# Kernel optimization log

Measured on AMD Instinct MI355X. Metric: run time of the kernel, lower is better.

## Reference

```python
import jax, jax.numpy as jnp
import numpy as np

B, C, H, W = 16, 512, 32, 32
G = min(C // 4, 32)  # group-norm groups = 32
EPS = 1e-6


def setup_inputs() -> dict:
    key = jax.random.key(0)
    ks = jax.random.split(key, 9)
    s = 1.0 / np.sqrt(C)
    return {
        "x": jax.random.normal(ks[0], (B, C, H, W), dtype=jnp.float32),
        "gn_gamma": jnp.ones((C,), jnp.float32),
        "gn_beta": jnp.zeros((C,), jnp.float32),
        "W0": jax.random.normal(ks[1], (C, C), jnp.float32) * s,
        "b0": jnp.zeros((C,), jnp.float32),
        "W1": jax.random.normal(ks[2], (C, C), jnp.float32) * s,
        "b1": jnp.zeros((C,), jnp.float32),
        "W2": jax.random.normal(ks[3], (C, C), jnp.float32) * s,
        "b2": jnp.zeros((C,), jnp.float32),
        "W3": jax.random.normal(ks[4], (C, C), jnp.float32) * s,
        "b3": jnp.zeros((C,), jnp.float32),
    }


def _group_norm(x, gamma, beta):
    b, c, h, w = x.shape
    xg = x.reshape(b, G, c // G, h, w)
    mu = jnp.mean(xg, axis=(2, 3, 4), keepdims=True)
    var = jnp.var(xg, axis=(2, 3, 4), keepdims=True)
    xn = ((xg - mu) * jax.lax.rsqrt(var + EPS)).reshape(b, c, h, w)
    return xn * gamma[None, :, None, None] + beta[None, :, None, None]


def _nin(x, Wm, bv):
    # 1x1 conv via channel contraction: bchw,cd->bdhw
    return jnp.einsum('bchw,cd->bdhw', x, Wm) + bv[None, :, None, None]


def reference(x, gn_gamma, gn_beta, W0, b0, W1, b1, W2, b2, W3, b3):
    b, c, h, w = x.shape
    hn = _group_norm(x, gn_gamma, gn_beta)
    q = _nin(hn, W0, b0)
    k = _nin(hn, W1, b1)
    v = _nin(hn, W2, b2)
    # attention scores over all spatial positions: [b, h, w, i, j]
    scores = jnp.einsum('bchw,bcij->bhwij', q, k) * (c ** -0.5)
    attn = jax.nn.softmax(scores.reshape(b, h, w, h * w), axis=-1).reshape(b, h, w, h, w)
    o = jnp.einsum('bhwij,bcij->bchw', attn, v)
    o = _nin(o, W3, b3)
    return x + o  # skip_rescale=False
```

## Files before the change

kernel.cpp:

```cpp
#include <hip/hip_runtime.h>
#include <stdint.h>

typedef __bf16 bf16_t;
typedef _Float16 f16_t;
typedef bf16_t bf16x8 __attribute__((ext_vector_type(8)));
typedef bf16_t bf16x4 __attribute__((ext_vector_type(4)));
typedef f16_t  f16x8  __attribute__((ext_vector_type(8)));
typedef f16_t  f16x4  __attribute__((ext_vector_type(4)));
typedef float floatx4 __attribute__((ext_vector_type(4)));

static constexpr int NB  = 16;
static constexpr int NC  = 512;
static constexpr int NHW = 1024;
static constexpr int NG  = 32;
static constexpr int CPG = 16;

#define SCALE 0.044194173824159216f
#define LOG2E 1.4426950408889634f

__global__ __launch_bounds__(256) void gn_stats_k(const float* __restrict__ x,
                                                  float* __restrict__ stats) {
  int bg = blockIdx.x;
  const float* xp = x + (size_t)bg * CPG * NHW;
  float s = 0.f, ss = 0.f;
  for (int i = threadIdx.x * 4; i < CPG * NHW; i += 256 * 4) {
    float4 v = *(const float4*)&xp[i];
    s += v.x + v.y + v.z + v.w;
    ss += v.x * v.x + v.y * v.y + v.z * v.z + v.w * v.w;
  }
#pragma unroll
  for (int off = 1; off < 64; off <<= 1) {
    s  += __shfl_xor(s,  off, 64);
    ss += __shfl_xor(ss, off, 64);
  }
  __shared__ float red[2][4];
  int wv = threadIdx.x >> 6;
  if ((threadIdx.x & 63) == 0) { red[0][wv] = s; red[1][wv] = ss; }
  __syncthreads();
  if (threadIdx.x == 0) {
    float st  = red[0][0] + red[0][1] + red[0][2] + red[0][3];
    float sst = red[1][0] + red[1][1] + red[1][2] + red[1][3];
    float mean = st * (1.f / 16384.f);
    float var  = sst * (1.f / 16384.f) - mean * mean;
    stats[bg * 2]     = mean;
    stats[bg * 2 + 1] = rsqrtf(var + 1e-6f);
  }
}

__global__ __launch_bounds__(256) void gn_apply_k(const float* __restrict__ x,
                                                  const float* __restrict__ gamma,
                                                  const float* __restrict__ beta,
                                                  const float* __restrict__ stats,
                                                  bf16_t* __restrict__ hnT,
                                                  bf16_t* __restrict__ hnN) {
  int bi = blockIdx.z;
  int c0 = blockIdx.y * 32;
  int n0 = blockIdx.x * 32;
  __shared__ float tile[32][33];
  int tn = threadIdx.x & 31;
  int tr = threadIdx.x >> 5;
  const float* xb = x + (size_t)bi * NC * NHW;
#pragma unroll
  for (int r = 0; r < 4; r++) {
    int c = c0 + tr + r * 8;
    int g = c >> 4;
    float mean = stats[(bi * NG + g) * 2];
    float rstd = stats[(bi * NG + g) * 2 + 1];
    float ga = gamma[c], be = beta[c];
    float v = xb[(size_t)c * NHW + n0 + tn];
    tile[tr + r * 8][tn] = (v - mean) * rstd * ga + be;
  }
  __syncthreads();
  int rl = threadIdx.x >> 3, ch = (threadIdx.x & 7) * 4;
  bf16_t* hb = hnT + (size_t)bi * NHW * NC;
  bf16x4 pk;
#pragma unroll
  for (int i = 0; i < 4; i++) pk[i] = (bf16_t)tile[ch + i][rl];
  *(bf16x4*)&hb[(size_t)(n0 + rl) * NC + c0 + ch] = pk;
  bf16_t* hc = hnN + (size_t)bi * NC * NHW;
  bf16x4 pk2;
#pragma unroll
  for (int i = 0; i < 4; i++) pk2[i] = (bf16_t)tile[rl][ch + i];
  *(bf16x4*)&hc[(size_t)(c0 + rl) * NHW + n0 + ch] = pk2;
}

__global__ __launch_bounds__(256) void wprep1_k(const float* __restrict__ W0,
                                                const float* __restrict__ W1,
                                                const float* __restrict__ W2,
                                                const float* __restrict__ W3,
                                                const float* __restrict__ b0,
                                                const float* __restrict__ b2,
                                                const float* __restrict__ b3,
                                                bf16_t* __restrict__ Wt,
                                                float* __restrict__ u,
                                                float* __restrict__ bb) {
  int z = blockIdx.z;
  if (z < 3) {
    const float* W = (z == 0) ? W0 : (z == 1) ? W1 : W2;
    bf16_t* o = Wt + (size_t)z * NC * NC;
    int d0 = blockIdx.x * 32, c0 = blockIdx.y * 32;
    int cl = threadIdx.x >> 3, dc = (threadIdx.x & 7) * 4;
    float4 v = *(const float4*)&W[(size_t)(c0 + cl) * NC + d0 + dc];
    bf16x4 pk;
    pk[0] = (bf16_t)v.x; pk[1] = (bf16_t)v.y; pk[2] = (bf16_t)v.z; pk[3] = (bf16_t)v.w;
    *(bf16x4*)&o[(size_t)(c0 + cl) * NC + d0 + dc] = pk;
    return;
  }
  if (z == 3) {
    bf16_t* o = Wt + (size_t)3 * NC * NC;
    int d0 = blockIdx.x * 32, c0 = blockIdx.y * 32;
    __shared__ float tile[32][33];
    int tdx = threadIdx.x & 31, tr = threadIdx.x >> 5;
#pragma unroll
    for (int r = 0; r < 4; r++)
      tile[tr + r * 8][tdx] = W3[(size_t)(c0 + tr + r * 8) * NC + d0 + tdx];
    __syncthreads();
    int dl = threadIdx.x >> 3, cc = (threadIdx.x & 7) * 4;
    bf16x4 pk;
#pragma unroll
    for (int i = 0; i < 4; i++) pk[i] = (bf16_t)tile[cc + i][dl];
    *(bf16x4*)&o[(size_t)(d0 + dl) * NC + c0 + cc] = pk;
    return;
  }
  int bx = blockIdx.x, by = blockIdx.y;
  if (by < 8) {
    int cblock = by * 16 + bx;
    int wv = threadIdx.x >> 6, lane = threadIdx.x & 63;
    int c = cblock * 4 + wv;
    const float* wr = W1 + (size_t)c * NC + lane * 8;
    float s = 0.f;
#pragma unroll
    for (int k = 0; k < 8; k++) s += wr[k] * b0[lane * 8 + k];
#pragma unroll
    for (int off = 1; off < 64; off <<= 1) s += __shfl_xor(s, off, 64);
    if (lane == 0) u[c] = SCALE * s;
    return;
  }
  if (by == 8 && bx < 8) {
    int e0 = bx * 64;
    int el = threadIdx.x & 63, sl = threadIdx.x >> 6;
    float s = 0.f;
    for (int d = sl * 128; d < sl * 128 + 128; d++)
      s += b2[d] * W3[(size_t)d * NC + e0 + el];
    __shared__ float red[4][64];
    red[sl][el] = s;
    __syncthreads();
    if (threadIdx.x < 64)
      bb[e0 + threadIdx.x] = red[0][threadIdx.x] + red[1][threadIdx.x] +
                             red[2][threadIdx.x] + red[3][threadIdx.x] + b3[e0 + threadIdx.x];
  }
}

__global__ __launch_bounds__(256) void w_k(const bf16_t* __restrict__ hnT,
                                           const float* __restrict__ u,
                                           float* __restrict__ w) {
  int row = blockIdx.x * 4 + (threadIdx.x >> 6);
  int lane = threadIdx.x & 63;
  bf16x8 h = *(const bf16x8*)&hnT[(size_t)row * NC + lane * 8];
  const float* up = u + lane * 8;
  float s = 0.f;
#pragma unroll
  for (int k = 0; k < 8; k++) s += (float)h[k] * up[k];
#pragma unroll
  for (int off = 1; off < 64; off <<= 1) s += __shfl_xor(s, off, 64);
  if (lane == 0) w[row] = s;
}

__device__ __forceinline__ void glds16(const bf16_t* g, bf16_t* lds) {
  __builtin_amdgcn_global_load_lds(
      (const __attribute__((address_space(1))) unsigned int*)g,
      (__attribute__((address_space(3))) unsigned int*)lds, 16, 0, 0);
}

__device__ __forceinline__ floatx4 mfma_bf16(bf16x8 a, bf16x8 b, floatx4 c) {
  return __builtin_amdgcn_mfma_f32_16x16x32_bf16(a, b, c, 0, 0, 0);
}

template<int KDIM, bool SWAP>
__device__ __forceinline__ void gemm_core(const bf16_t* __restrict__ A,
                                          const bf16_t* __restrict__ B,
                                          int m0, int n0,
                                          floatx4 (&acc)[4][4]) {
  __shared__ bf16_t As[128 * 64];
  __shared__ bf16_t Bs[128 * 64];
  const int tid = threadIdx.x, lane = tid & 63, wv = tid >> 6;
  const int l16 = lane & 15, quad = lane >> 4;
  const int wm = wv & 1, wn = wv >> 1;
  const int x7 = l16 & 7;

  const int srow = lane >> 3;
  const int schunk = (lane & 7) ^ srow;
  const bf16_t* aptr = A + (size_t)(m0 + wv * 32 + srow) * KDIM + schunk * 8;
  const bf16_t* bptr = B + (size_t)(n0 + wv * 32 + srow) * KDIM + schunk * 8;
  bf16_t* as_ = &As[(wv * 32) * 64];
  bf16_t* bs_ = &Bs[(wv * 32) * 64];

  for (int k0 = 0; k0 < KDIM; k0 += 64) {
    __syncthreads();
#pragma unroll
    for (int i = 0; i < 4; i++) {
      glds16(aptr + (size_t)(8 * i) * KDIM, as_ + (8 * i) * 64);
      glds16(bptr + (size_t)(8 * i) * KDIM, bs_ + (8 * i) * 64);
    }
    aptr += 64; bptr += 64;
    __syncthreads();
    bf16x8 af[2][4], bfv[2][4];
#pragma unroll
    for (int h = 0; h < 2; h++)
#pragma unroll
      for (int i = 0; i < 4; i++) {
        int q = h * 4 + quad;
        af[h][i]  = *(const bf16x8*)&As[(wm * 64 + i * 16 + l16) * 64 + ((q ^ x7) * 8)];
        bfv[h][i] = *(const bf16x8*)&Bs[(wn * 64 + i * 16 + l16) * 64 + ((q ^ x7) * 8)];
      }
#pragma unroll
    for (int h = 0; h < 2; h++)
#pragma unroll
      for (int i = 0; i < 4; i++)
#pragma unroll
        for (int j = 0; j < 4; j++)
          acc[i][j] = SWAP ? mfma_bf16(bfv[h][j], af[h][i], acc[i][j])
                           : mfma_bf16(af[h][i], bfv[h][j], acc[i][j]);
  }
}

#define ACC_INIT(acc)                                   \
  floatx4 acc[4][4];                                    \
  _Pragma("unroll") for (int i = 0; i < 4; i++)         \
  _Pragma("unroll") for (int j = 0; j < 4; j++)         \
    acc[i][j] = (floatx4){0.f, 0.f, 0.f, 0.f};

__global__ __launch_bounds__(256) void wprep2_k(const bf16_t* __restrict__ Wt,
                                                bf16_t* __restrict__ Mt,
                                                bf16_t* __restrict__ W23t) {
  int z = blockIdx.z;
  const bf16_t* A = (z == 0) ? (Wt + (size_t)1 * NC * NC) : (Wt + (size_t)3 * NC * NC);
  const bf16_t* B = (z == 0) ? (Wt + (size_t)0 * NC * NC) : (Wt + (size_t)2 * NC * NC);
  bf16_t* out = (z == 0) ? Mt : W23t;
  const float sc = (z == 0) ? SCALE : 1.f;
  int n0 = blockIdx.x * 128, m0 = blockIdx.y * 128;
  ACC_INIT(acc);
  gemm_core<NC, false>(A, B, m0, n0, acc);
  const int lane = threadIdx.x & 63, wv = threadIdx.x >> 6;
  const int l16 = lane & 15, quad = lane >> 4, wm = wv & 1, wn = wv >> 1;
#pragma unroll
  for (int i = 0; i < 4; i++)
#pragma unroll
    for (int j = 0; j < 4; j++) {
      int row = m0 + wm * 64 + i * 16 + quad * 4;
      int col = n0 + wn * 64 + j * 16 + l16;
#pragma unroll
      for (int r = 0; r < 4; r++)
        out[(size_t)(row + r) * NC + col] = (bf16_t)(acc[i][j][r] * sc);
    }
}

__global__ __launch_bounds__(256) void gemm_g_k(const bf16_t* __restrict__ hnT,
                                                const bf16_t* __restrict__ Mt,
                                                bf16_t* __restrict__ G) {
  int n0 = blockIdx.x * 128, m0 = blockIdx.y * 128;
  ACC_INIT(acc);
  gemm_core<NC, true>(hnT, Mt, m0, n0, acc);
  const int lane = threadIdx.x & 63, wv = threadIdx.x >> 6;
  const int l16 = lane & 15, quad = lane >> 4, wm = wv & 1, wn = wv >> 1;
#pragma unroll
  for (int i = 0; i < 4; i++) {
    int m = m0 + wm * 64 + i * 16 + l16;
#pragma unroll
    for (int j = 0; j < 4; j++) {
      int eb = n0 + wn * 64 + j * 16 + quad * 4;
      bf16x4 pk;
#pragma unroll
      for (int r = 0; r < 4; r++) pk[r] = (bf16_t)(acc[i][j][r]);
      *(bf16x4*)&G[(size_t)m * NC + eb] = pk;
    }
  }
}

__global__ __launch_bounds__(256) void gemm_s_k(const bf16_t* __restrict__ G,
                                                const bf16_t* __restrict__ hnT,
                                                f16_t* __restrict__ S) {
  int bi = blockIdx.z;
  int n0 = blockIdx.x * 128, m0 = blockIdx.y * 128;
  const bf16_t* A = G + (size_t)bi * NHW * NC;
  const bf16_t* B = hnT + (size_t)bi * NHW * NC;
  ACC_INIT(acc);
  gemm_core<NC, true>(A, B, m0, n0, acc);

  const int lane = threadIdx.x & 63, wv = threadIdx.x >> 6;
  const int l16 = lane & 15, quad = lane >> 4, wm = wv & 1, wn = wv >> 1;
  f16_t* out = S + (size_t)bi * NHW * NHW;
#pragma unroll
  for (int i = 0; i < 4; i++) {
    int m = m0 + wm * 64 + i * 16 + l16;
#pragma unroll
    for (int j = 0; j < 4; j++) {
      int nb = n0 + wn * 64 + j * 16 + quad * 4;
      f16x4 pk;
#pragma unroll
      for (int r = 0; r < 4; r++) pk[r] = (f16_t)(acc[i][j][r]);
      *(f16x4*)&out[(size_t)m * NHW + nb] = pk;
    }
  }
}

__global__ __launch_bounds__(256) void softmax_k(const f16_t* __restrict__ S,
                                                 const float* __restrict__ w,
                                                 bf16_t* __restrict__ P) {
  int row = blockIdx.x * 4 + (threadIdx.x >> 6);
  int lane = threadIdx.x & 63;
  int b = row >> 10;
  const f16_t* sp = S + (size_t)row * NHW + lane * 16;
  const float* wp = w + b * NHW + lane * 16;
  f16x8 a = *(const f16x8*)sp;
  f16x8 bq = *(const f16x8*)(sp + 8);
  float v[16];
#pragma unroll
  for (int k = 0; k < 8; k++) { v[k] = (float)a[k] + wp[k]; v[8 + k] = (float)bq[k] + wp[8 + k]; }
  float mx = v[0];
#pragma unroll
  for (int k = 1; k < 16; k++) mx = fmaxf(mx, v[k]);
#pragma unroll
  for (int off = 1; off < 64; off <<= 1) mx = fmaxf(mx, __shfl_xor(mx, off, 64));
  float e[16], s = 0.f;
#pragma unroll
  for (int k = 0; k < 16; k++) { e[k] = exp2f((v[k] - mx) * LOG2E); s += e[k]; }
#pragma unroll
  for (int off = 1; off < 64; off <<= 1) s += __shfl_xor(s, off, 64);
  float inv = 1.f / s;
  bf16x8 o0, o1;
#pragma unroll
  for (int k = 0; k < 8; k++) { o0[k] = (bf16_t)(e[k] * inv); o1[k] = (bf16_t)(e[8 + k] * inv); }
  bf16_t* pp = P + (size_t)row * NHW + lane * 16;
  *(bf16x8*)pp = o0;
  *(bf16x8*)(pp + 8) = o1;
}

__global__ __launch_bounds__(256) void gemm_t_k(const bf16_t* __restrict__ P,
                                                const bf16_t* __restrict__ hnN,
                                                bf16_t* __restrict__ T) {
  int bi = blockIdx.z;
  int n0 = blockIdx.x * 128, m0 = blockIdx.y * 128;
  const bf16_t* A = P + (size_t)bi * NHW * NHW;
  const bf16_t* B = hnN + (size_t)bi * NC * NHW;
  ACC_INIT(acc);
  gemm_core<NHW, true>(A, B, m0, n0, acc);

  const int lane = threadIdx.x & 63, wv = threadIdx.x >> 6;
  const int l16 = lane & 15, quad = lane >> 4, wm = wv & 1, wn = wv >> 1;
  bf16_t* out = T + (size_t)bi * NHW * NC;
#pragma unroll
  for (int i = 0; i < 4; i++) {
    int m = m0 + wm * 64 + i * 16 + l16;
#pragma unroll
    for (int j = 0; j < 4; j++) {
      int cb = n0 + wn * 64 + j * 16 + quad * 4;
      bf16x4 pk;
#pragma unroll
      for (int r = 0; r < 4; r++) pk[r] = (bf16_t)(acc[i][j][r]);
      *(bf16x4*)&out[(size_t)m * NC + cb] = pk;
    }
  }
}

__global__ __launch_bounds__(256) void gemm_out_k(const bf16_t* __restrict__ T,
                                                  const bf16_t* __restrict__ W23t,
                                                  const float* __restrict__ bb,
                                                  const float* __restrict__ x,
                                                  float* __restrict__ outp) {
  int bi = blockIdx.z;
  int n0 = blockIdx.x * 128, m0 = blockIdx.y * 128;
  const bf16_t* A = T + (size_t)bi * NHW * NC;
  ACC_INIT(acc);
  gemm_core<NC, false>(A, W23t, m0, n0, acc);

  const int lane = threadIdx.x & 63, wv = threadIdx.x >> 6;
  const int l16 = lane & 15, quad = lane >> 4, wm = wv & 1, wn = wv >> 1;
  const float* xb = x + (size_t)bi * NC * NHW;
  float* ob = outp + (size_t)bi * NC * NHW;
#pragma unroll
  for (int i = 0; i < 4; i++)
#pragma unroll
    for (int j = 0; j < 4; j++) {
      int row = m0 + wm * 64 + i * 16 + quad * 4;
      int col = n0 + wn * 64 + j * 16 + l16;
      float bv = bb[col];
      size_t base = (size_t)col * NHW + row;
      float4 xv = *(const float4*)&xb[base];
      float4 pk;
      pk.x = acc[i][j][0] + bv + xv.x;
      pk.y = acc[i][j][1] + bv + xv.y;
      pk.z = acc[i][j][2] + bv + xv.z;
      pk.w = acc[i][j][3] + bv + xv.w;
      *(float4*)&ob[base] = pk;
    }
}

extern "C" void kernel_launch(void* const* d_in, const int* in_sizes, int n_in,
                              void* d_out, int out_size, void* d_ws, size_t ws_size,
                              hipStream_t stream) {
  (void)in_sizes; (void)n_in; (void)out_size; (void)ws_size;
  const float* x     = (const float*)d_in[0];
  const float* gamma = (const float*)d_in[1];
  const float* beta  = (const float*)d_in[2];
  const float* W0    = (const float*)d_in[3];
  const float* b0    = (const float*)d_in[4];
  const float* W1    = (const float*)d_in[5];
  const float* b1    = (const float*)d_in[6];  (void)b1;
  const float* W2    = (const float*)d_in[7];
  const float* b2    = (const float*)d_in[8];
  const float* W3    = (const float*)d_in[9];
  const float* b3    = (const float*)d_in[10];
  float* outp = (float*)d_out;

  char* ws = (char*)d_ws;
  const size_t PLANE = (size_t)NB * NHW * NC * sizeof(bf16_t);
  float* stats = (float*)ws;
  size_t off = 4096;
  bf16_t* hnT = (bf16_t*)(ws + off); off += PLANE;
  bf16_t* hnN = (bf16_t*)(ws + off); off += PLANE;
  bf16_t* G   = (bf16_t*)(ws + off); off += PLANE;
  bf16_t* Wt  = (bf16_t*)(ws + off); off += 4 * (size_t)NC * NC * sizeof(bf16_t);
  bf16_t* Mt   = (bf16_t*)(ws + off); off += (size_t)NC * NC * sizeof(bf16_t);
  bf16_t* W23t = (bf16_t*)(ws + off); off += (size_t)NC * NC * sizeof(bf16_t);
  float*  u   = (float*)(ws + off);  off += 2048;
  float*  bb  = (float*)(ws + off);  off += 2048;
  float*  w   = (float*)(ws + off);  off += (size_t)NB * NHW * sizeof(float);
  f16_t*  S   = (f16_t*)(ws + off);  off += (size_t)NB * NHW * NHW * sizeof(f16_t);
  bf16_t* P   = (bf16_t*)S;
  bf16_t* T   = G;

  gn_stats_k<<<NB * NG, 256, 0, stream>>>(x, stats);
  gn_apply_k<<<dim3(32, 16, NB), 256, 0, stream>>>(x, gamma, beta, stats, hnT, hnN);
  wprep1_k<<<dim3(16, 16, 5), 256, 0, stream>>>(W0, W1, W2, W3, b0, b2, b3, Wt, u, bb);
  wprep2_k<<<dim3(4, 4, 2), 256, 0, stream>>>(Wt, Mt, W23t);
  w_k<<<dim3(NB * NHW / 4), 256, 0, stream>>>(hnT, u, w);
  gemm_g_k<<<dim3(4, 128), 256, 0, stream>>>(hnT, Mt, G);
  gemm_s_k<<<dim3(8, 8, NB), 256, 0, stream>>>(G, hnT, S);
  softmax_k<<<dim3(NB * NHW / 4), 256, 0, stream>>>(S, w, P);
  gemm_t_k<<<dim3(4, 8, NB), 256, 0, stream>>>(P, hnN, T);
  gemm_out_k<<<dim3(4, 8, NB), 256, 0, stream>>>(T, W23t, bb, x, outp);
}
```

Baseline: 245.6 us.

## Fuse prep kernels and fold key-bias term into G epilogue, dropping w_k

The group-norm stats kernel is merged into the weight-prep launch, and the group-norm apply is merged with the weight-product GEMM, so independent small kernels share one launch each. The separate w_k pass and the per-column w add in softmax are removed. Instead, the bias vector u is added to G in the gemm_g epilogue, so the S GEMM produces the u·hn_j term directly. This cuts launches and one full read of hnT. In exchange, u is now rounded to bf16 inside G, and the merged prep2 kernel carries GEMM-sized LDS, which may lower occupancy for its group-norm blocks.

```diff
diff --git a/kernel.cpp b/kernel.cpp
--- a/kernel.cpp
+++ b/kernel.cpp
@@ -18,83 +18,110 @@
 #define SCALE 0.044194173824159216f
 #define LOG2E 1.4426950408889634f
 
-__global__ __launch_bounds__(256) void gn_stats_k(const float* __restrict__ x,
-                                                  float* __restrict__ stats) {
-  int bg = blockIdx.x;
-  const float* xp = x + (size_t)bg * CPG * NHW;
-  float s = 0.f, ss = 0.f;
-  for (int i = threadIdx.x * 4; i < CPG * NHW; i += 256 * 4) {
-    float4 v = *(const float4*)&xp[i];
-    s += v.x + v.y + v.z + v.w;
-    ss += v.x * v.x + v.y * v.y + v.z * v.z + v.w * v.w;
-  }
-#pragma unroll
-  for (int off = 1; off < 64; off <<= 1) {
-    s  += __shfl_xor(s,  off, 64);
-    ss += __shfl_xor(ss, off, 64);
-  }
-  __shared__ float red[2][4];
-  int wv = threadIdx.x >> 6;
-  if ((threadIdx.x & 63) == 0) { red[0][wv] = s; red[1][wv] = ss; }
-  __syncthreads();
-  if (threadIdx.x == 0) {
-    float st  = red[0][0] + red[0][1] + red[0][2] + red[0][3];
-    float sst = red[1][0] + red[1][1] + red[1][2] + red[1][3];
-    float mean = st * (1.f / 16384.f);
-    float var  = sst * (1.f / 16384.f) - mean * mean;
-    stats[bg * 2]     = mean;
-    stats[bg * 2 + 1] = rsqrtf(var + 1e-6f);
-  }
-}
-
-__global__ __launch_bounds__(256) void gn_apply_k(const float* __restrict__ x,
-                                                  const float* __restrict__ gamma,
-                                                  const float* __restrict__ beta,
-                                                  const float* __restrict__ stats,
-                                                  bf16_t* __restrict__ hnT,
-                                                  bf16_t* __restrict__ hnN) {
-  int bi = blockIdx.z;
-  int c0 = blockIdx.y * 32;
-  int n0 = blockIdx.x * 32;
-  __shared__ float tile[32][33];
-  int tn = threadIdx.x & 31;
-  int tr = threadIdx.x >> 5;
-  const float* xb = x + (size_t)bi * NC * NHW;
-#pragma unroll
-  for (int r = 0; r < 4; r++) {
-    int c = c0 + tr + r * 8;
-    int g = c >> 4;
-    float mean = stats[(bi * NG + g) * 2];
-    float rstd = stats[(bi * NG + g) * 2 + 1];
-    float ga = gamma[c], be = beta[c];
-    float v = xb[(size_t)c * NHW + n0 + tn];
-    tile[tr + r * 8][tn] = (v - mean) * rstd * ga + be;
-  }
-  __syncthreads();
-  int rl = threadIdx.x >> 3, ch = (threadIdx.x & 7) * 4;
-  bf16_t* hb = hnT + (size_t)bi * NHW * NC;
-  bf16x4 pk;
-#pragma unroll
-  for (int i = 0; i < 4; i++) pk[i] = (bf16_t)tile[ch + i][rl];
-  *(bf16x4*)&hb[(size_t)(n0 + rl) * NC + c0 + ch] = pk;
-  bf16_t* hc = hnN + (size_t)bi * NC * NHW;
-  bf16x4 pk2;
-#pragma unroll
-  for (int i = 0; i < 4; i++) pk2[i] = (bf16_t)tile[rl][ch + i];
-  *(bf16x4*)&hc[(size_t)(c0 + rl) * NHW + n0 + ch] = pk2;
-}
-
-__global__ __launch_bounds__(256) void wprep1_k(const float* __restrict__ W0,
-                                                const float* __restrict__ W1,
-                                                const float* __restrict__ W2,
-                                                const float* __restrict__ W3,
-                                                const float* __restrict__ b0,
-                                                const float* __restrict__ b2,
-                                                const float* __restrict__ b3,
-                                                bf16_t* __restrict__ Wt,
-                                                float* __restrict__ u,
-                                                float* __restrict__ bb) {
+__device__ __forceinline__ void glds16(const bf16_t* g, bf16_t* lds) {
+  __builtin_amdgcn_global_load_lds(
+      (const __attribute__((address_space(1))) unsigned int*)g,
+      (__attribute__((address_space(3))) unsigned int*)lds, 16, 0, 0);
+}
+
+__device__ __forceinline__ floatx4 mfma_bf16(bf16x8 a, bf16x8 b, floatx4 c) {
+  return __builtin_amdgcn_mfma_f32_16x16x32_bf16(a, b, c, 0, 0, 0);
+}
+
+template<int KDIM, bool SWAP>
+__device__ __forceinline__ void gemm_core(const bf16_t* __restrict__ A,
+                                          const bf16_t* __restrict__ B,
+                                          int m0, int n0,
+                                          floatx4 (&acc)[4][4],
+                                          bf16_t* As, bf16_t* Bs) {
+  const int tid = threadIdx.x, lane = tid & 63, wv = tid >> 6;
+  const int l16 = lane & 15, quad = lane >> 4;
+  const int wm = wv & 1, wn = wv >> 1;
+  const int x7 = l16 & 7;
+
+  const int srow = lane >> 3;
+  const int schunk = (lane & 7) ^ srow;
+  const bf16_t* aptr = A + (size_t)(m0 + wv * 32 + srow) * KDIM + schunk * 8;
+  const bf16_t* bptr = B + (size_t)(n0 + wv * 32 + srow) * KDIM + schunk * 8;
+  bf16_t* as_ = &As[(wv * 32) * 64];
+  bf16_t* bs_ = &Bs[(wv * 32) * 64];
+
+  for (int k0 = 0; k0 < KDIM; k0 += 64) {
+    __syncthreads();
+#pragma unroll
+    for (int i = 0; i < 4; i++) {
+      glds16(aptr + (size_t)(8 * i) * KDIM, as_ + (8 * i) * 64);
+      glds16(bptr + (size_t)(8 * i) * KDIM, bs_ + (8 * i) * 64);
+    }
+    aptr += 64; bptr += 64;
+    __syncthreads();
+    bf16x8 af[2][4], bfv[2][4];
+#pragma unroll
+    for (int h = 0; h < 2; h++)
+#pragma unroll
+      for (int i = 0; i < 4; i++) {
+        int q = h * 4 + quad;
+        af[h][i]  = *(const bf16x8*)&As[(wm * 64 + i * 16 + l16) * 64 + ((q ^ x7) * 8)];
+        bfv[h][i] = *(const bf16x8*)&Bs[(wn * 64 + i * 16 + l16) * 64 + ((q ^ x7) * 8)];
+      }
+#pragma unroll
+    for (int h = 0; h < 2; h++)
+#pragma unroll
+      for (int i = 0; i < 4; i++)
+#pragma unroll
+        for (int j = 0; j < 4; j++)
+          acc[i][j] = SWAP ? mfma_bf16(bfv[h][j], af[h][i], acc[i][j])
+                           : mfma_bf16(af[h][i], bfv[h][j], acc[i][j]);
+  }
+}
+
+#define ACC_INIT(acc)                                   \
+  floatx4 acc[4][4];                                    \
+  _Pragma("unroll") for (int i = 0; i < 4; i++)         \
+  _Pragma("unroll") for (int j = 0; j < 4; j++)         \
+    acc[i][j] = (floatx4){0.f, 0.f, 0.f, 0.f};
+
+__global__ __launch_bounds__(256) void prep1_k(const float* __restrict__ x,
+                                               const float* __restrict__ W0,
+                                               const float* __restrict__ W1,
+                                               const float* __restrict__ W2,
+                                               const float* __restrict__ W3,
+                                               const float* __restrict__ b0,
+                                               const float* __restrict__ b2,
+                                               const float* __restrict__ b3,
+                                               bf16_t* __restrict__ Wt,
+                                               float* __restrict__ u,
+                                               float* __restrict__ bb,
+                                               float* __restrict__ stats) {
   int z = blockIdx.z;
+  if (z >= 5) {
+    int bg = (z - 5) * 256 + blockIdx.y * 16 + blockIdx.x;
+    const float* xp = x + (size_t)bg * CPG * NHW;
+    float s = 0.f, ss = 0.f;
+    for (int i = threadIdx.x * 4; i < CPG * NHW; i += 256 * 4) {
+      float4 v = *(const float4*)&xp[i];
+      s += v.x + v.y + v.z + v.w;
+      ss += v.x * v.x + v.y * v.y + v.z * v.z + v.w * v.w;
+    }
+#pragma unroll
+    for (int off = 1; off < 64; off <<= 1) {
+      s  += __shfl_xor(s,  off, 64);
+      ss += __shfl_xor(ss, off, 64);
+    }
+    __shared__ float red2[2][4];
+    int wv = threadIdx.x >> 6;
+    if ((threadIdx.x & 63) == 0) { red2[0][wv] = s; red2[1][wv] = ss; }
+    __syncthreads();
+    if (threadIdx.x == 0) {
+      float st  = red2[0][0] + red2[0][1] + red2[0][2] + red2[0][3];
+      float sst = red2[1][0] + red2[1][1] + red2[1][2] + red2[1][3];
+      float mean = st * (1.f / 16384.f);
+      float var  = sst * (1.f / 16384.f) - mean * mean;
+      stats[bg * 2]     = mean;
+      stats[bg * 2 + 1] = rsqrtf(var + 1e-6f);
+    }
+    return;
+  }
   if (z < 3) {
     const float* W = (z == 0) ? W0 : (z == 1) ? W1 : W2;
     bf16_t* o = Wt + (size_t)z * NC * NC;
@@ -151,96 +178,59 @@
   }
 }
 
-__global__ __launch_bounds__(256) void w_k(const bf16_t* __restrict__ hnT,
-                                           const float* __restrict__ u,
-                                           float* __restrict__ w) {
-  int row = blockIdx.x * 4 + (threadIdx.x >> 6);
-  int lane = threadIdx.x & 63;
-  bf16x8 h = *(const bf16x8*)&hnT[(size_t)row * NC + lane * 8];
-  const float* up = u + lane * 8;
-  float s = 0.f;
-#pragma unroll
-  for (int k = 0; k < 8; k++) s += (float)h[k] * up[k];
-#pragma unroll
-  for (int off = 1; off < 64; off <<= 1) s += __shfl_xor(s, off, 64);
-  if (lane == 0) w[row] = s;
-}
-
-__device__ __forceinline__ void glds16(const bf16_t* g, bf16_t* lds) {
-  __builtin_amdgcn_global_load_lds(
-      (const __attribute__((address_space(1))) unsigned int*)g,
-      (__attribute__((address_space(3))) unsigned int*)lds, 16, 0, 0);
-}
-
-__device__ __forceinline__ floatx4 mfma_bf16(bf16x8 a, bf16x8 b, floatx4 c) {
-  return __builtin_amdgcn_mfma_f32_16x16x32_bf16(a, b, c, 0, 0, 0);
-}
-
-template<int KDIM, bool SWAP>
-__device__ __forceinline__ void gemm_core(const bf16_t* __restrict__ A,
-                                          const bf16_t* __restrict__ B,
-                                          int m0, int n0,
-                                          floatx4 (&acc)[4][4]) {
+__global__ __launch_bounds__(256) void prep2_k(const float* __restrict__ x,
+                                               const float* __restrict__ gamma,
+                                               const float* __restrict__ beta,
+                                               const float* __restrict__ stats,
+                                               const bf16_t* __restrict__ Wt,
+                                               bf16_t* __restrict__ hnT,
+                                               bf16_t* __restrict__ hnN,
+                                               bf16_t* __restrict__ Mt,
+                                               bf16_t* __restrict__ W23t) {
   __shared__ bf16_t As[128 * 64];
+  __shared__ float tile[32][33];
+  int z = blockIdx.z;
+  if (z < NB) {
+    int bi = z;
+    int c0 = blockIdx.y * 32;
+    int n0 = blockIdx.x * 32;
+    int tn = threadIdx.x & 31;
+    int tr = threadIdx.x >> 5;
+    const float* xb = x + (size_t)bi * NC * NHW;
+#pragma unroll
+    for (int r = 0; r < 4; r++) {
+      int c = c0 + tr + r * 8;
+      int g = c >> 4;
+      float mean = stats[(bi * NG + g) * 2];
+      float rstd = stats[(bi * NG + g) * 2 + 1];
+      float ga = gamma[c], be = beta[c];
+      float v = xb[(size_t)c * NHW + n0 + tn];
+      tile[tr + r * 8][tn] = (v - mean) * rstd * ga + be;
+    }
+    __syncthreads();
+    int rl = threadIdx.x >> 3, ch = (threadIdx.x & 7) * 4;
+    bf16_t* hb = hnT + (size_t)bi * NHW * NC;
+    bf16x4 pk;
+#pragma unroll
+    for (int i = 0; i < 4; i++) pk[i] = (bf16_t)tile[ch + i][rl];
+    *(bf16x4*)&hb[(size_t)(n0 + rl) * NC + c0 + ch] = pk;
+    bf16_t* hc = hnN + (size_t)bi * NC * NHW;
+    bf16x4 pk2;
+#pragma unroll
+    for (int i = 0; i < 4; i++) pk2[i] = (bf16_t)tile[rl][ch + i];
+    *(bf16x4*)&hc[(size_t)(c0 + rl) * NHW + n0 + ch] = pk2;
+    return;
+  }
+  if (blockIdx.y >= 4 || blockIdx.x >= 8) return;
   __shared__ bf16_t Bs[128 * 64];
-  const int tid = threadIdx.x, lane = tid & 63, wv = tid >> 6;
-  const int l16 = lane & 15, quad = lane >> 4;
-  const int wm = wv & 1, wn = wv >> 1;
-  const int x7 = l16 & 7;
-
-  const int srow = lane >> 3;
-  const int schunk = (lane & 7) ^ srow;
-  const bf16_t* aptr = A + (size_t)(m0 + wv * 32 + srow) * KDIM + schunk * 8;
-  const bf16_t* bptr = B + (size_t)(n0 + wv * 32 + srow) * KDIM + schunk * 8;
-  bf16_t* as_ = &As[(wv * 32) * 64];
-  bf16_t* bs_ = &Bs[(wv * 32) * 64];
-
-  for (int k0 = 0; k0 < KDIM; k0 += 64) {
-    __syncthreads();
-#pragma unroll
-    for (int i = 0; i < 4; i++) {
-      glds16(aptr + (size_t)(8 * i) * KDIM, as_ + (8 * i) * 64);
-      glds16(bptr + (size_t)(8 * i) * KDIM, bs_ + (8 * i) * 64);
-    }
-    aptr += 64; bptr += 64;
-    __syncthreads();
-    bf16x8 af[2][4], bfv[2][4];
-#pragma unroll
-    for (int h = 0; h < 2; h++)
-#pragma unroll
-      for (int i = 0; i < 4; i++) {
-        int q = h * 4 + quad;
-        af[h][i]  = *(const bf16x8*)&As[(wm * 64 + i * 16 + l16) * 64 + ((q ^ x7) * 8)];
-        bfv[h][i] = *(const bf16x8*)&Bs[(wn * 64 + i * 16 + l16) * 64 + ((q ^ x7) * 8)];
-      }
-#pragma unroll
-    for (int h = 0; h < 2; h++)
-#pragma unroll
-      for (int i = 0; i < 4; i++)
-#pragma unroll
-        for (int j = 0; j < 4; j++)
-          acc[i][j] = SWAP ? mfma_bf16(bfv[h][j], af[h][i], acc[i][j])
-                           : mfma_bf16(af[h][i], bfv[h][j], acc[i][j]);
-  }
-}
-
-#define ACC_INIT(acc)                                   \
-  floatx4 acc[4][4];                                    \
-  _Pragma("unroll") for (int i = 0; i < 4; i++)         \
-  _Pragma("unroll") for (int j = 0; j < 4; j++)         \
-    acc[i][j] = (floatx4){0.f, 0.f, 0.f, 0.f};
-
-__global__ __launch_bounds__(256) void wprep2_k(const bf16_t* __restrict__ Wt,
-                                                bf16_t* __restrict__ Mt,
-                                                bf16_t* __restrict__ W23t) {
-  int z = blockIdx.z;
-  const bf16_t* A = (z == 0) ? (Wt + (size_t)1 * NC * NC) : (Wt + (size_t)3 * NC * NC);
-  const bf16_t* B = (z == 0) ? (Wt + (size_t)0 * NC * NC) : (Wt + (size_t)2 * NC * NC);
-  bf16_t* out = (z == 0) ? Mt : W23t;
-  const float sc = (z == 0) ? SCALE : 1.f;
-  int n0 = blockIdx.x * 128, m0 = blockIdx.y * 128;
+  int zz = blockIdx.x >> 2;
+  int n0 = (blockIdx.x & 3) * 128, m0 = blockIdx.y * 128;
+  const bf16_t* A = (zz == 0) ? (Wt + (size_t)1 * NC * NC) : (Wt + (size_t)3 * NC * NC);
+  const bf16_t* B = (zz == 0) ? (Wt + (size_t)0 * NC * NC) : (Wt + (size_t)2 * NC * NC);
+  bf16_t* out = (zz == 0) ? Mt : W23t;
+  const float sc = (zz == 0) ? SCALE : 1.f;
   ACC_INIT(acc);
-  gemm_core<NC, false>(A, B, m0, n0, acc);
+  gemm_core<NC, false>(A, B, m0, n0, acc, As, Bs);
   const int lane = threadIdx.x & 63, wv = threadIdx.x >> 6;
   const int l16 = lane & 15, quad = lane >> 4, wm = wv & 1, wn = wv >> 1;
 #pragma unroll
@@ -257,10 +247,13 @@
 
 __global__ __launch_bounds__(256) void gemm_g_k(const bf16_t* __restrict__ hnT,
                                                 const bf16_t* __restrict__ Mt,
+                                                const float* __restrict__ u,
                                                 bf16_t* __restrict__ G) {
+  __shared__ bf16_t As[128 * 64];
+  __shared__ bf16_t Bs[128 * 64];
   int n0 = blockIdx.x * 128, m0 = blockIdx.y * 128;
   ACC_INIT(acc);
-  gemm_core<NC, true>(hnT, Mt, m0, n0, acc);
+  gemm_core<NC, true>(hnT, Mt, m0, n0, acc, As, Bs);
   const int lane = threadIdx.x & 63, wv = threadIdx.x >> 6;
   const int l16 = lane & 15, quad = lane >> 4, wm = wv & 1, wn = wv >> 1;
 #pragma unroll
@@ -269,9 +262,12 @@
 #pragma unroll
     for (int j = 0; j < 4; j++) {
       int eb = n0 + wn * 64 + j * 16 + quad * 4;
+      float4 uv = *(const float4*)&u[eb];
       bf16x4 pk;
-#pragma unroll
-      for (int r = 0; r < 4; r++) pk[r] = (bf16_t)(acc[i][j][r]);
+      pk[0] = (bf16_t)(acc[i][j][0] + uv.x);
+      pk[1] = (bf16_t)(acc[i][j][1] + uv.y);
+      pk[2] = (bf16_t)(acc[i][j][2] + uv.z);
+      pk[3] = (bf16_t)(acc[i][j][3] + uv.w);
       *(bf16x4*)&G[(size_t)m * NC + eb] = pk;
     }
   }
@@ -280,12 +276,14 @@
 __global__ __launch_bounds__(256) void gemm_s_k(const bf16_t* __restrict__ G,
                                                 const bf16_t* __restrict__ hnT,
                                                 f16_t* __restrict__ S) {
+  __shared__ bf16_t As[128 * 64];
+  __shared__ bf16_t Bs[128 * 64];
   int bi = blockIdx.z;
   int n0 = blockIdx.x * 128, m0 = blockIdx.y * 128;
   const bf16_t* A = G + (size_t)bi * NHW * NC;
   const bf16_t* B = hnT + (size_t)bi * NHW * NC;
   ACC_INIT(acc);
-  gemm_core<NC, true>(A, B, m0, n0, acc);
+  gemm_core<NC, true>(A, B, m0, n0, acc, As, Bs);
 
   const int lane = threadIdx.x & 63, wv = threadIdx.x >> 6;
   const int l16 = lane & 15, quad = lane >> 4, wm = wv & 1, wn = wv >> 1;
@@ -305,18 +303,15 @@
 }
 
 __global__ __launch_bounds__(256) void softmax_k(const f16_t* __restrict__ S,
-                                                 const float* __restrict__ w,
                                                  bf16_t* __restrict__ P) {
   int row = blockIdx.x * 4 + (threadIdx.x >> 6);
   int lane = threadIdx.x & 63;
-  int b = row >> 10;
   const f16_t* sp = S + (size_t)row * NHW + lane * 16;
-  const float* wp = w + b * NHW + lane * 16;
   f16x8 a = *(const f16x8*)sp;
   f16x8 bq = *(const f16x8*)(sp + 8);
   float v[16];
 #pragma unroll
-  for (int k = 0; k < 8; k++) { v[k] = (float)a[k] + wp[k]; v[8 + k] = (float)bq[k] + wp[8 + k]; }
+  for (int k = 0; k < 8; k++) { v[k] = (float)a[k]; v[8 + k] = (float)bq[k]; }
   float mx = v[0];
 #pragma unroll
   for (int k = 1; k < 16; k++) mx = fmaxf(mx, v[k]);
@@ -339,12 +334,14 @@
 __global__ __launch_bounds__(256) void gemm_t_k(const bf16_t* __restrict__ P,
                                                 const bf16_t* __restrict__ hnN,
                                                 bf16_t* __restrict__ T) {
+  __shared__ bf16_t As[128 * 64];
+  __shared__ bf16_t Bs[128 * 64];
   int bi = blockIdx.z;
   int n0 = blockIdx.x * 128, m0 = blockIdx.y * 128;
   const bf16_t* A = P + (size_t)bi * NHW * NHW;
   const bf16_t* B = hnN + (size_t)bi * NC * NHW;
   ACC_INIT(acc);
-  gemm_core<NHW, true>(A, B, m0, n0, acc);
+  gemm_core<NHW, true>(A, B, m0, n0, acc, As, Bs);
 
   const int lane = threadIdx.x & 63, wv = threadIdx.x >> 6;
   const int l16 = lane & 15, quad = lane >> 4, wm = wv & 1, wn = wv >> 1;
@@ -368,11 +365,13 @@
                                                   const float* __restrict__ bb,
                                                   const float* __restrict__ x,
                                                   float* __restrict__ outp) {
+  __shared__ bf16_t As[128 * 64];
+  __shared__ bf16_t Bs[128 * 64];
   int bi = blockIdx.z;
   int n0 = blockIdx.x * 128, m0 = blockIdx.y * 128;
   const bf16_t* A = T + (size_t)bi * NHW * NC;
   ACC_INIT(acc);
-  gemm_core<NC, false>(A, W23t, m0, n0, acc);
+  gemm_core<NC, false>(A, W23t, m0, n0, acc, As, Bs);
 
   const int lane = threadIdx.x & 63, wv = threadIdx.x >> 6;
   const int l16 = lane & 15, quad = lane >> 4, wm = wv & 1, wn = wv >> 1;
@@ -425,19 +424,15 @@
   bf16_t* W23t = (bf16_t*)(ws + off); off += (size_t)NC * NC * sizeof(bf16_t);
   float*  u   = (float*)(ws + off);  off += 2048;
   float*  bb  = (float*)(ws + off);  off += 2048;
-  float*  w   = (float*)(ws + off);  off += (size_t)NB * NHW * sizeof(float);
   f16_t*  S   = (f16_t*)(ws + off);  off += (size_t)NB * NHW * NHW * sizeof(f16_t);
   bf16_t* P   = (bf16_t*)S;
   bf16_t* T   = G;
 
-  gn_stats_k<<<NB * NG, 256, 0, stream>>>(x, stats);
-  gn_apply_k<<<dim3(32, 16, NB), 256, 0, stream>>>(x, gamma, beta, stats, hnT, hnN);
-  wprep1_k<<<dim3(16, 16, 5), 256, 0, stream>>>(W0, W1, W2, W3, b0, b2, b3, Wt, u, bb);
-  wprep2_k<<<dim3(4, 4, 2), 256, 0, stream>>>(Wt, Mt, W23t);
-  w_k<<<dim3(NB * NHW / 4), 256, 0, stream>>>(hnT, u, w);
-  gemm_g_k<<<dim3(4, 128), 256, 0, stream>>>(hnT, Mt, G);
+  prep1_k<<<dim3(16, 16, 7), 256, 0, stream>>>(x, W0, W1, W2, W3, b0, b2, b3, Wt, u, bb, stats);
+  prep2_k<<<dim3(32, 16, NB + 1), 256, 0, stream>>>(x, gamma, beta, stats, Wt, hnT, hnN, Mt, W23t);
+  gemm_g_k<<<dim3(4, 128), 256, 0, stream>>>(hnT, Mt, u, G);
   gemm_s_k<<<dim3(8, 8, NB), 256, 0, stream>>>(G, hnT, S);
-  softmax_k<<<dim3(NB * NHW / 4), 256, 0, stream>>>(S, w, P);
+  softmax_k<<<dim3(NB * NHW / 4), 256, 0, stream>>>(S, P);
   gemm_t_k<<<dim3(4, 8, NB), 256, 0, stream>>>(P, hnN, T);
   gemm_out_k<<<dim3(4, 8, NB), 256, 0, stream>>>(T, W23t, bb, x, outp);
 }
```

Measured after the change: 243.4 us (median of 2 runs). No clear change (-0.9%).
